# Kernel optimization log

Hardware: AMD Instinct MI355X
Metric: run time of the kernel (lower is better)

The kernel has to match this reference:

```python
import jax, jax.numpy as jnp
import numpy as np
from itertools import product

B, C, HH, WW, DD, N = 2, 32, 96, 96, 96, 30000


def setup_inputs() -> dict:
    key = jax.random.key(0)
    k1, k2, k3 = jax.random.split(key, 3)
    voxel_features = jax.random.normal(k1, (B, C, HH, WW, DD), dtype=jnp.float32)
    # vertices in normalized [-1, 1] grid_sample coordinates (x, y, z)
    vertices = jax.random.uniform(k2, (B, N, 3), dtype=jnp.float32, minval=-1.0, maxval=1.0)
    fan_in = C * 27
    conv_w = jax.random.normal(k3, (C, C, 1, 27), dtype=jnp.float32) * np.sqrt(2.0 / fan_in)
    conv_b = jnp.zeros((C,), dtype=jnp.float32)
    return {
        "voxel_features": voxel_features,
        "vertices": vertices,
        "conv_w": conv_w,
        "conv_b": conv_b,
        "img_H": HH,
        "img_W": WW,
        "img_D": DD,
    }


def _trilinear_sample(voxel_features, grid):
    """grid_sample(mode='bilinear', padding_mode='border', align_corners=True).
    voxel_features: (B,C,H,W,D); grid: (B,N,K,3) with (x,y,z) in [-1,1],
    x -> D axis, y -> W axis, z -> H axis. Returns (B,C,N,K)."""
    b, c, h, w, d = voxel_features.shape
    x, y, z = grid[..., 0], grid[..., 1], grid[..., 2]
    ix = jnp.clip((x + 1.0) * 0.5 * (d - 1), 0.0, d - 1)
    iy = jnp.clip((y + 1.0) * 0.5 * (w - 1), 0.0, w - 1)
    iz = jnp.clip((z + 1.0) * 0.5 * (h - 1), 0.0, h - 1)
    x0 = jnp.floor(ix).astype(jnp.int32); x1 = jnp.minimum(x0 + 1, d - 1)
    y0 = jnp.floor(iy).astype(jnp.int32); y1 = jnp.minimum(y0 + 1, w - 1)
    z0 = jnp.floor(iz).astype(jnp.int32); z1 = jnp.minimum(z0 + 1, h - 1)
    fx = ix - x0; fy = iy - y0; fz = iz - z0
    vf = voxel_features.reshape(b, c, h * w * d)
    n, k = grid.shape[1], grid.shape[2]

    def gather(zi, yi, xi):
        lin = (zi * w + yi) * d + xi  # (B,N,K)
        g = jnp.take_along_axis(vf, lin.reshape(b, 1, n * k), axis=2)
        return g.reshape(b, c, n, k)

    def wgt(wz, wy, wx):
        return (wz * wy * wx)[:, None]  # (B,1,N,K)

    out = (
        gather(z0, y0, x0) * wgt(1 - fz, 1 - fy, 1 - fx)
        + gather(z0, y0, x1) * wgt(1 - fz, 1 - fy, fx)
        + gather(z0, y1, x0) * wgt(1 - fz, fy, 1 - fx)
        + gather(z0, y1, x1) * wgt(1 - fz, fy, fx)
        + gather(z1, y0, x0) * wgt(fz, 1 - fy, 1 - fx)
        + gather(z1, y0, x1) * wgt(fz, 1 - fy, fx)
        + gather(z1, y1, x0) * wgt(fz, fy, 1 - fx)
        + gather(z1, y1, x1) * wgt(fz, fy, fx)
    )
    return out


def reference(voxel_features, vertices, conv_w, conv_b, img_H, img_W, img_D):
    # 27 neighbor offsets in normalized coords, scaled per (x,y,z) component
    offs = jnp.asarray(list(product((-1, 0, 1), repeat=3)), dtype=jnp.float32)  # (27,3)
    scale = jnp.array(
        [2.0 / (img_D - 1), 2.0 / (img_W - 1), 2.0 / (img_H - 1)], dtype=jnp.float32
    )
    shift = offs * scale  # (27,3)
    grid = vertices[:, :, None, :] + shift[None, None]  # (B,N,27,3)
    feats = _trilinear_sample(voxel_features, grid)  # (B,C,N,27)
    # Conv2d(C,C,(1,27)): weighted reduction over (C_in, 27) -> (B,N,C_out)
    out = jnp.einsum("bink,oik->bno", feats, conv_w[:, :, 0, :]) + conv_b
    return out
```

## Files before the change

### kernel.cpp

```cpp
#include <hip/hip_runtime.h>
#include <stdint.h>

#define HWD 884736ull
#define NV 30000
#define AST 1032

typedef __attribute__((ext_vector_type(8))) __bf16 bf16x8;
typedef __attribute__((ext_vector_type(4))) float f32x4;
typedef __attribute__((ext_vector_type(4))) unsigned int uint4v;

__device__ __forceinline__ unsigned short f2bf(float f) {
    union { float f; unsigned int u; } v; v.f = f;
    unsigned int u = v.u;
    return (unsigned short)((u + 0x7FFFu + ((u >> 16) & 1u)) >> 16);
}

__device__ __forceinline__ float bf2f(unsigned short s) {
    union { unsigned int u; float f; } v;
    v.u = ((unsigned int)s) << 16;
    return v.f;
}

__device__ __forceinline__ void axis_setup(float coord, float sc, int& wstart, float w[3][4]) {
    int i0[3], i1[3];
    float fr[3];
#pragma unroll
    for (int a = 0; a < 3; ++a) {
        float g = coord + (float)(a - 1) * sc;
        float ix = (g + 1.0f) * 0.5f * 95.0f;
        ix = fminf(fmaxf(ix, 0.0f), 95.0f);
        float fl = floorf(ix);
        int x0 = (int)fl;
        i0[a] = x0;
        i1[a] = min(x0 + 1, 95);
        fr[a] = ix - fl;
    }
    int ws = min(max(i0[1] - 1, 0), 92);
    wstart = ws;
#pragma unroll
    for (int a = 0; a < 3; ++a) {
        int d0 = min(max(i0[a] - ws, 0), 3);
        int d1 = min(max(i1[a] - ws, 0), 3);
        float f1 = fr[a], f0 = 1.0f - f1;
#pragma unroll
        for (int j = 0; j < 4; ++j)
            w[a][j] = (d0 == j ? f0 : 0.0f) + (d1 == j ? f1 : 0.0f);
    }
}

__global__ __launch_bounds__(256) void prep_kernel(const float* __restrict__ cw,
                                                   unsigned short* __restrict__ Wp) {
    int gid = blockIdx.x * 256 + threadIdx.x;
    int j = gid & 7;
    int l = (gid >> 3) & 63;
    int t = (gid >> 9) & 1;
    int s = gid >> 10;
    int kk = ((l >> 4) & 3) * 8 + j;
    int o = t * 16 + (l & 15);
    float v = 0.0f;
    if (kk < 27) v = cw[(size_t)o * 864 + s * 27 + kk];
    Wp[gid] = f2bf(v);
}

__global__ __launch_bounds__(256) void transpose_kernel(const float* __restrict__ vox,
                                                        unsigned short* __restrict__ voxT) {
    int blk = blockIdx.x;
    int tid = threadIdx.x;
    int b = blk / 9216;
    int zy = blk % 9216;
    const float* src = vox + (size_t)b * 32 * HWD + (size_t)zy * 96;
    unsigned short* dst = voxT + (size_t)blk * 3072;
#pragma unroll
    for (int i = 0; i < 3; ++i) {
        int idx = i * 256 + tid;
        int c = idx & 31;
        int x4 = idx >> 5;
        f32x4 v = *(const f32x4*)(src + (size_t)c * HWD + x4 * 4);
#pragma unroll
        for (int k = 0; k < 4; ++k)
            dst[(x4 * 4 + k) * 32 + c] = f2bf(v[k]);
    }
}

__global__ __launch_bounds__(512) void fused_kernel(const unsigned short* __restrict__ voxT,
                                                    const float* __restrict__ verts,
                                                    const unsigned short* __restrict__ Wp,
                                                    const float* __restrict__ bias,
                                                    float* __restrict__ out) {
    __shared__ unsigned short At[16 * AST];
    int tid = threadIdx.x;
    int vl = tid >> 5;
    int c = tid & 31;
    int vg = (int)blockIdx.x * 16 + vl;

    const float* vp = verts + (size_t)vg * 3;
    float vx = vp[0], vy = vp[1], vz = vp[2];
    const float sc = 2.0f / 95.0f;
    int wsx, wsy, wsz;
    float wx[3][4], wy[3][4], wz[3][4];
    axis_setup(vx, sc, wsx, wx);
    axis_setup(vy, sc, wsy, wy);
    axis_setup(vz, sc, wsz, wz);
    int bb = (vg >= NV) ? 1 : 0;
    const unsigned short* vb = voxT + (size_t)bb * HWD * 32 + c;

    float f[27];
#pragma unroll
    for (int k = 0; k < 27; ++k) f[k] = 0.0f;

#pragma unroll
    for (int tz = 0; tz < 4; ++tz) {
        float rx[4][3];
#pragma unroll
        for (int ty = 0; ty < 4; ++ty) {
            const unsigned short* row =
                vb + (((size_t)(wsz + tz) * 96 + (size_t)(wsy + ty)) * 96 + wsx) * 32;
            float b0 = bf2f(row[0]);
            float b1 = bf2f(row[32]);
            float b2 = bf2f(row[64]);
            float b3 = bf2f(row[96]);
#pragma unroll
            for (int a = 0; a < 3; ++a)
                rx[ty][a] = b0 * wx[a][0] + b1 * wx[a][1] + b2 * wx[a][2] + b3 * wx[a][3];
        }
        float ry[3][3];
#pragma unroll
        for (int b = 0; b < 3; ++b)
#pragma unroll
            for (int a = 0; a < 3; ++a)
                ry[b][a] = rx[0][a] * wy[b][0] + rx[1][a] * wy[b][1] +
                           rx[2][a] * wy[b][2] + rx[3][a] * wy[b][3];
#pragma unroll
        for (int g = 0; g < 3; ++g)
#pragma unroll
            for (int b = 0; b < 3; ++b)
#pragma unroll
                for (int a = 0; a < 3; ++a)
                    f[9 * a + 3 * b + g] += wz[g][tz] * ry[b][a];
    }

    unsigned int pk[16];
#pragma unroll
    for (int i = 0; i < 16; ++i) {
        float lo = (2 * i < 27) ? f[2 * i] : 0.0f;
        float hi = (2 * i + 1 < 27) ? f[2 * i + 1] : 0.0f;
        pk[i] = (unsigned int)f2bf(lo) | ((unsigned int)f2bf(hi) << 16);
    }
    uint4v* dst = (uint4v*)&At[vl * AST + c * 32];
    uint4v s0 = {pk[0], pk[1], pk[2], pk[3]};
    uint4v s1 = {pk[4], pk[5], pk[6], pk[7]};
    uint4v s2 = {pk[8], pk[9], pk[10], pk[11]};
    uint4v s3 = {pk[12], pk[13], pk[14], pk[15]};
    dst[0] = s0; dst[1] = s1; dst[2] = s2; dst[3] = s3;

    __syncthreads();

    int wv = tid >> 6;
    if (wv < 2) {
        int lane = tid & 63;
        int mrow = lane & 15, quad = lane >> 4;
        const bf16x8* wp = (const bf16x8*)Wp;
        const unsigned short* arow = &At[mrow * AST + quad * 8];
        f32x4 acc = {0.f, 0.f, 0.f, 0.f};
#pragma unroll 8
        for (int s = 0; s < 32; ++s) {
            bf16x8 a = *(const bf16x8*)(arow + s * 32);
            bf16x8 b = wp[(s * 2 + wv) * 64 + lane];
            acc = __builtin_amdgcn_mfma_f32_16x16x32_bf16(a, b, acc, 0, 0, 0);
        }
        float bs = bias[wv * 16 + mrow];
#pragma unroll
        for (int r = 0; r < 4; ++r) {
            int v = (int)blockIdx.x * 16 + quad * 4 + r;
            out[(size_t)v * 32 + wv * 16 + mrow] = acc[r] + bs;
        }
    }
}

extern "C" void kernel_launch(void* const* d_in, const int* in_sizes, int n_in,
                              void* d_out, int out_size, void* d_ws, size_t ws_size,
                              hipStream_t stream) {
    const float* vox = (const float*)d_in[0];
    const float* verts = (const float*)d_in[1];
    const float* cw = (const float*)d_in[2];
    const float* cb = (const float*)d_in[3];
    float* out = (float*)d_out;

    unsigned short* Wp = (unsigned short*)d_ws;
    unsigned short* voxT = (unsigned short*)((char*)d_ws + 65536);

    hipLaunchKernelGGL(prep_kernel, dim3(128), dim3(256), 0, stream, cw, Wp);
    hipLaunchKernelGGL(transpose_kernel, dim3(18432), dim3(256), 0, stream, vox, voxT);
    hipLaunchKernelGGL(fused_kernel, dim3(3750), dim3(512), 0, stream,
                       voxT, verts, Wp, cb, out);
}
```

Before: 420.4 us.

## Stage transpose through LDS and process two channels per thread in gather

The transpose kernel now loads two rows of 96 voxels into shared memory with nontemporal loads and writes the channels-last bf16 output as coalesced 16-byte stores, replacing the scattered 2-byte global stores. The fused gather kernel has each thread handle a channel pair with 32-bit loads and packed float2 math, halving the block to 256 threads. It also accumulates the y-axis reduction inside the load loop and XOR-swizzles the LDS A-tile layout to avoid bank conflicts in the MFMA reads. This adds register pressure per thread and an extra LDS round-trip in the transpose.

```diff
diff --git a/kernel.cpp b/kernel.cpp
--- a/kernel.cpp
+++ b/kernel.cpp
@@ -7,6 +7,7 @@
 
 typedef __attribute__((ext_vector_type(8))) __bf16 bf16x8;
 typedef __attribute__((ext_vector_type(4))) float f32x4;
+typedef __attribute__((ext_vector_type(2))) float f32x2;
 typedef __attribute__((ext_vector_type(4))) unsigned int uint4v;
 
 __device__ __forceinline__ unsigned short f2bf(float f) {
@@ -19,6 +20,14 @@
     union { unsigned int u; float f; } v;
     v.u = ((unsigned int)s) << 16;
     return v.f;
+}
+
+__device__ __forceinline__ f32x2 up2(unsigned int u) {
+    union { unsigned int u; float f; } lo, hi;
+    lo.u = u << 16;
+    hi.u = u & 0xFFFF0000u;
+    f32x2 r; r.x = lo.f; r.y = hi.f;
+    return r;
 }
 
 __device__ __forceinline__ void axis_setup(float coord, float sc, int& wstart, float w[3][4]) {
@@ -64,33 +73,43 @@
 
 __global__ __launch_bounds__(256) void transpose_kernel(const float* __restrict__ vox,
                                                         unsigned short* __restrict__ voxT) {
+    __shared__ unsigned short T[192 * 40];
     int blk = blockIdx.x;
     int tid = threadIdx.x;
-    int b = blk / 9216;
-    int zy = blk % 9216;
-    const float* src = vox + (size_t)b * 32 * HWD + (size_t)zy * 96;
-    unsigned short* dst = voxT + (size_t)blk * 3072;
+    int b = blk / 4608;
+    int zy = blk - b * 4608;
+    const float* src = vox + (size_t)b * 32 * HWD + (size_t)zy * 192;
+#pragma unroll
+    for (int i = 0; i < 6; ++i) {
+        int j = i * 256 + tid;
+        int c = j & 31;
+        int x4 = j >> 5;
+        f32x4 v = __builtin_nontemporal_load((const f32x4*)(src + (size_t)c * HWD + x4 * 4));
+#pragma unroll
+        for (int k = 0; k < 4; ++k)
+            T[(x4 * 4 + k) * 40 + c] = f2bf(v[k]);
+    }
+    __syncthreads();
+    unsigned short* dst = voxT + (size_t)blk * 6144;
 #pragma unroll
     for (int i = 0; i < 3; ++i) {
-        int idx = i * 256 + tid;
-        int c = idx & 31;
-        int x4 = idx >> 5;
-        f32x4 v = *(const f32x4*)(src + (size_t)c * HWD + x4 * 4);
-#pragma unroll
-        for (int k = 0; k < 4; ++k)
-            dst[(x4 * 4 + k) * 32 + c] = f2bf(v[k]);
-    }
-}
-
-__global__ __launch_bounds__(512) void fused_kernel(const unsigned short* __restrict__ voxT,
+        int q = i * 256 + tid;
+        int x = q >> 2;
+        int cg = (q & 3) * 8;
+        uint4v val = *(const uint4v*)&T[x * 40 + cg];
+        *(uint4v*)(dst + q * 8) = val;
+    }
+}
+
+__global__ __launch_bounds__(256) void fused_kernel(const unsigned short* __restrict__ voxT,
                                                     const float* __restrict__ verts,
                                                     const unsigned short* __restrict__ Wp,
                                                     const float* __restrict__ bias,
                                                     float* __restrict__ out) {
     __shared__ unsigned short At[16 * AST];
     int tid = threadIdx.x;
-    int vl = tid >> 5;
-    int c = tid & 31;
+    int vl = tid >> 4;
+    int cp = tid & 15;
     int vg = (int)blockIdx.x * 16 + vl;
 
     const float* vp = verts + (size_t)vg * 3;
@@ -102,56 +121,76 @@
     axis_setup(vy, sc, wsy, wy);
     axis_setup(vz, sc, wsz, wz);
     int bb = (vg >= NV) ? 1 : 0;
-    const unsigned short* vb = voxT + (size_t)bb * HWD * 32 + c;
-
-    float f[27];
-#pragma unroll
-    for (int k = 0; k < 27; ++k) f[k] = 0.0f;
+    const unsigned short* vb = voxT + (size_t)bb * HWD * 32 + 2 * cp;
+
+    f32x2 zz = {0.f, 0.f};
+    f32x2 f[27];
+#pragma unroll
+    for (int k = 0; k < 27; ++k) f[k] = zz;
 
 #pragma unroll
     for (int tz = 0; tz < 4; ++tz) {
-        float rx[4][3];
+        f32x2 ry[3][3];
+#pragma unroll
+        for (int bq = 0; bq < 3; ++bq)
+#pragma unroll
+            for (int a = 0; a < 3; ++a) ry[bq][a] = zz;
 #pragma unroll
         for (int ty = 0; ty < 4; ++ty) {
             const unsigned short* row =
                 vb + (((size_t)(wsz + tz) * 96 + (size_t)(wsy + ty)) * 96 + wsx) * 32;
-            float b0 = bf2f(row[0]);
-            float b1 = bf2f(row[32]);
-            float b2 = bf2f(row[64]);
-            float b3 = bf2f(row[96]);
-#pragma unroll
-            for (int a = 0; a < 3; ++a)
-                rx[ty][a] = b0 * wx[a][0] + b1 * wx[a][1] + b2 * wx[a][2] + b3 * wx[a][3];
+            unsigned int u0 = *(const unsigned int*)(row);
+            unsigned int u1 = *(const unsigned int*)(row + 32);
+            unsigned int u2 = *(const unsigned int*)(row + 64);
+            unsigned int u3 = *(const unsigned int*)(row + 96);
+            f32x2 b0 = up2(u0), b1 = up2(u1), b2 = up2(u2), b3 = up2(u3);
+#pragma unroll
+            for (int a = 0; a < 3; ++a) {
+                f32x2 r = b0 * wx[a][0] + b1 * wx[a][1] + b2 * wx[a][2] + b3 * wx[a][3];
+#pragma unroll
+                for (int bq = 0; bq < 3; ++bq)
+                    ry[bq][a] += r * wy[bq][ty];
+            }
         }
-        float ry[3][3];
-#pragma unroll
-        for (int b = 0; b < 3; ++b)
-#pragma unroll
-            for (int a = 0; a < 3; ++a)
-                ry[b][a] = rx[0][a] * wy[b][0] + rx[1][a] * wy[b][1] +
-                           rx[2][a] * wy[b][2] + rx[3][a] * wy[b][3];
 #pragma unroll
         for (int g = 0; g < 3; ++g)
 #pragma unroll
-            for (int b = 0; b < 3; ++b)
+            for (int bq = 0; bq < 3; ++bq)
 #pragma unroll
                 for (int a = 0; a < 3; ++a)
-                    f[9 * a + 3 * b + g] += wz[g][tz] * ry[b][a];
-    }
-
-    unsigned int pk[16];
+                    f[9 * a + 3 * bq + g] += wz[g][tz] * ry[bq][a];
+    }
+
+    unsigned int pk0[16], pk1[16];
 #pragma unroll
     for (int i = 0; i < 16; ++i) {
-        float lo = (2 * i < 27) ? f[2 * i] : 0.0f;
-        float hi = (2 * i + 1 < 27) ? f[2 * i + 1] : 0.0f;
-        pk[i] = (unsigned int)f2bf(lo) | ((unsigned int)f2bf(hi) << 16);
-    }
-    uint4v* dst = (uint4v*)&At[vl * AST + c * 32];
-    uint4v s0 = {pk[0], pk[1], pk[2], pk[3]};
-    uint4v s1 = {pk[4], pk[5], pk[6], pk[7]};
-    uint4v s2 = {pk[8], pk[9], pk[10], pk[11]};
-    uint4v s3 = {pk[12], pk[13], pk[14], pk[15]};
-    dst[0] = s0; dst[1] = s1; dst[2] = s2; dst[3] = s3;
+        float l0 = (2 * i < 27) ? f[2 * i].x : 0.0f;
+        float h0 = (2 * i + 1 < 27) ? f[2 * i + 1].x : 0.0f;
+        float l1 = (2 * i < 27) ? f[2 * i].y : 0.0f;
+        float h1 = (2 * i + 1 < 27) ? f[2 * i + 1].y : 0.0f;
+        pk0[i] = (unsigned int)f2bf(l0) | ((unsigned int)f2bf(h0) << 16);
+        pk1[i] = (unsigned int)f2bf(l1) | ((unsigned int)f2bf(h1) << 16);
+    }
+    unsigned short* abase = &At[vl * AST + cp * 64];
+    int e = cp & 7;
+    {
+        uint4v c0 = {pk0[0], pk0[1], pk0[2], pk0[3]};
+        uint4v c1 = {pk0[4], pk0[5], pk0[6], pk0[7]};
+        uint4v c2 = {pk0[8], pk0[9], pk0[10], pk0[11]};
+        uint4v c3 = {pk0[12], pk0[13], pk0[14], pk0[15]};
+        uint4v c4 = {pk1[0], pk1[1], pk1[2], pk1[3]};
+        uint4v c5 = {pk1[4], pk1[5], pk1[6], pk1[7]};
+        uint4v c6 = {pk1[8], pk1[9], pk1[10], pk1[11]};
+        uint4v c7 = {pk1[12], pk1[13], pk1[14], pk1[15]};
+        *(uint4v*)(abase + ((0 ^ e) << 3)) = c0;
+        *(uint4v*)(abase + ((1 ^ e) << 3)) = c1;
+        *(uint4v*)(abase + ((2 ^ e) << 3)) = c2;
+        *(uint4v*)(abase + ((3 ^ e) << 3)) = c3;
+        *(uint4v*)(abase + ((4 ^ e) << 3)) = c4;
+        *(uint4v*)(abase + ((5 ^ e) << 3)) = c5;
+        *(uint4v*)(abase + ((6 ^ e) << 3)) = c6;
+        *(uint4v*)(abase + ((7 ^ e) << 3)) = c7;
+    }
 
     __syncthreads();
 
@@ -160,11 +199,12 @@
         int lane = tid & 63;
         int mrow = lane & 15, quad = lane >> 4;
         const bf16x8* wp = (const bf16x8*)Wp;
-        const unsigned short* arow = &At[mrow * AST + quad * 8];
         f32x4 acc = {0.f, 0.f, 0.f, 0.f};
 #pragma unroll 8
         for (int s = 0; s < 32; ++s) {
-            bf16x8 a = *(const bf16x8*)(arow + s * 32);
+            int cpg = s >> 1;
+            int kk = ((s & 1) << 2) | quad;
+            bf16x8 a = *(const bf16x8*)&At[mrow * AST + cpg * 64 + ((kk ^ (cpg & 7)) << 3)];
             bf16x8 b = wp[(s * 2 + wv) * 64 + lane];
             acc = __builtin_amdgcn_mfma_f32_16x16x32_bf16(a, b, acc, 0, 0, 0);
         }
@@ -190,7 +230,7 @@
     unsigned short* voxT = (unsigned short*)((char*)d_ws + 65536);
 
     hipLaunchKernelGGL(prep_kernel, dim3(128), dim3(256), 0, stream, cw, Wp);
-    hipLaunchKernelGGL(transpose_kernel, dim3(18432), dim3(256), 0, stream, vox, voxT);
-    hipLaunchKernelGGL(fused_kernel, dim3(3750), dim3(512), 0, stream,
+    hipLaunchKernelGGL(transpose_kernel, dim3(9216), dim3(256), 0, stream, vox, voxT);
+    hipLaunchKernelGGL(fused_kernel, dim3(3750), dim3(256), 0, stream,
                        voxT, verts, Wp, cb, out);
 }
```

Result: faster. 397.0 us (-5.6%).
